# Kernel tuning notes

Hardware: AMD Instinct MI355X
Metric: run time of the kernel (lower is better)

The kernel has to match this reference:

```python
import jax, jax.numpy as jnp
import numpy as np

B, O, L, E = 8, 4, 1024, 1024
BETA = 512
NSEG = 12
OUT = 1


def setup_inputs() -> dict:
    key = jax.random.key(0)
    ks = jax.random.split(key, 8)
    hidden = jax.random.normal(ks[0], (B, O, L, E), jnp.float32)
    # strictly increasing boundaries in (1, L), shared across the O options (as in the torch code)
    raw = jnp.sort(jax.random.randint(ks[1], (B, NSEG), 2, L - NSEG), axis=-1)
    idx = raw + jnp.arange(NSEG, dtype=raw.dtype)
    s = 0.02
    Wp = jax.random.normal(ks[2], (E, 2 * BETA), jnp.float32) * s
    bp = jnp.zeros((2 * BETA,), jnp.float32)
    Wa0 = jax.random.normal(ks[3], (2 * BETA, BETA), jnp.float32) * s
    ba0 = jnp.zeros((BETA,), jnp.float32)
    Wa = jax.random.normal(ks[4], (BETA, BETA), jnp.float32) * s
    ba = jnp.zeros((BETA,), jnp.float32)
    Wl0 = jax.random.normal(ks[5], (8 * BETA, BETA), jnp.float32) * s
    bl0 = jnp.zeros((BETA,), jnp.float32)
    Wl = jax.random.normal(ks[6], (BETA, OUT), jnp.float32) * s
    bl = jnp.zeros((OUT,), jnp.float32)
    return dict(hidden=hidden, idx=idx, Wp=Wp, bp=bp, Wa0=Wa0, ba0=ba0,
                Wa=Wa, ba=ba, Wl0=Wl0, bl0=bl0, Wl=Wl, bl=bl)


def _seg_mean(P, starts, ends):
    # P: [B,O,L+1,E] exclusive prefix sums; starts/ends: [B,K] token offsets.
    s = jnp.take_along_axis(P, starts[:, None, :, None], axis=2)
    e = jnp.take_along_axis(P, ends[:, None, :, None], axis=2)
    cnt = (ends - starts).astype(P.dtype)[:, None, :, None]
    return (e - s) / cnt  # [B,O,K,E]


def _get_param(x, Wp, bp):
    e = 1.0 + jax.nn.relu(x @ Wp + bp)
    a, b = jnp.split(e, 2, axis=-1)
    return a, b


def _attn_pool(a, b, Wa0, ba0, Wa, ba):
    # attention-weighted reduction over axis -2 (the 'logic' operator)
    h = jax.nn.relu(jnp.concatenate([a, b], axis=-1) @ Wa0 + ba0)
    w = jax.nn.softmax(h @ Wa + ba, axis=-2)
    return (w * a).sum(axis=-2), (w * b).sum(axis=-2)


def reference(hidden, idx, Wp, bp, Wa0, ba0, Wa, ba, Wl0, bl0, Wl, bl):
    # ---- init_embed: ragged segment means via prefix sums (one pass, no host syncs)
    P = jnp.concatenate([jnp.zeros_like(hidden[:, :, :1]),
                         jnp.cumsum(hidden, axis=2)], axis=2)  # [B,O,L+1,E]
    ones = jnp.ones((idx.shape[0], 1), idx.dtype)
    starts_c = jnp.concatenate([ones, idx[:, :NSEG - 3]], axis=1)  # [B, NSEG-2]
    ends_c = idx[:, :NSEG - 2]
    ctx = _seg_mean(P, starts_c, ends_c)                                # [B,O,Nc,E]
    q = _seg_mean(P, idx[:, NSEG - 3:NSEG - 2], idx[:, NSEG - 2:NSEG - 1])[:, :, 0]
    o = _seg_mean(P, idx[:, NSEG - 2:NSEG - 1], idx[:, NSEG - 1:NSEG])[:, :, 0]
    allc = _seg_mean(P, ones, idx[:, NSEG - 3:NSEG - 2])[:, :, 0]       # [B,O,E]
    # ---- beta params for context segments
    a_c, b_c = _get_param(ctx, Wp, bp)                                  # [B,O,Nc,BETA]
    # intersection over segments
    ia, ib = _attn_pool(a_c, b_c, Wa0, ba0, Wa, ba)                     # [B,O,BETA]
    # renew: pair each segment with the intersection, pool over the pair axis
    pa = jnp.stack([a_c, jnp.broadcast_to(ia[:, :, None, :], a_c.shape)], axis=-2)
    pb = jnp.stack([b_c, jnp.broadcast_to(ib[:, :, None, :], b_c.shape)], axis=-2)
    na, nb = _attn_pool(pa, pb, Wa0, ba0, Wa, ba)                       # [B,O,Nc,BETA]
    # union: invert, attention-pool over segments, invert back
    ua, ub = _attn_pool(1.0 / na, 1.0 / nb, Wa0, ba0, Wa, ba)
    ua, ub = 1.0 / ua, 1.0 / ub                                         # [B,O,BETA]
    # ---- beta params for question / option / whole-context spans
    a_q, b_q = _get_param(q, Wp, bp)
    a_o, b_o = _get_param(o, Wp, bp)
    a_ac, b_ac = _get_param(allc, Wp, bp)
    # ---- classify head: concat 4 beta embeddings -> 8*BETA -> MLP -> logits
    cat = jnp.concatenate([ua, ub, a_ac, b_ac, a_o, b_o, a_q, b_q], axis=-1)
    h = jax.nn.relu(cat @ Wl0 + bl0)
    return h @ Wl + bl  # [B,O,OUT]
```

## Files before the change

### kernel.cpp

```cpp
#include <hip/hip_runtime.h>
#include <hip/hip_bf16.h>

#define B_    8
#define O_    4
#define L_    1024
#define E_    1024
#define BETA_ 512
#define NSEG_ 12
#define BO_   32
#define NCH_  16

enum : size_t {
  WS_SPART = 0,
  WS_X     = WS_SPART + (size_t)BO_ * NCH_ * 12 * E_,
  WS_P1P   = WS_X     + (size_t)BO_ * 13 * E_,
  WS_H1P   = WS_P1P   + (size_t)8  * BO_ * 13 * E_,
  WS_T1P   = WS_H1P   + (size_t)16 * BO_ * 10 * BETA_,
  WS_H2P   = WS_T1P   + (size_t)8  * BO_ * 10 * BETA_,
  WS_T2P   = WS_H2P   + (size_t)8  * BO_ * BETA_,
  WS_H3P   = WS_T2P   + (size_t)8  * BO_ * BETA_,
  WS_T3P   = WS_H3P   + (size_t)16 * BO_ * 10 * BETA_,
  WS_HFP   = WS_T3P   + (size_t)8  * BO_ * 10 * BETA_,
  WS_TE    = WS_HFP   + (size_t)32 * BO_ * BETA_,
  WS_T1B   = WS_TE    + (size_t)BO_ * 13 * E_,
  WS_IAB   = WS_T1B   + (size_t)BO_ * 10 * BETA_,
  WS_RN    = WS_IAB   + (size_t)BO_ * 2 * BETA_,
  WS_CAT   = WS_RN    + (size_t)BO_ * 10 * E_,
  WS_END   = WS_CAT   + (size_t)BO_ * 8 * BETA_,
};

__device__ __forceinline__ float relu_(float v) { return v > 0.f ? v : 0.f; }

__global__ void k1_segsum(const float* __restrict__ hidden, const int* __restrict__ idx,
                          float* __restrict__ Spart) {
    const int chunk = blockIdx.x;
    const int bo = blockIdx.y;
    const int b = bo >> 2;
    int cuts[13];
    cuts[0] = 1;
#pragma unroll
    for (int i = 0; i < 12; ++i) cuts[i + 1] = idx[b * NSEG_ + i];
    const int e4 = threadIdx.x << 2;
    float* sp = Spart + ((size_t)(bo * NCH_ + chunk) * 12) * E_ + e4;
    const float4 z = make_float4(0.f, 0.f, 0.f, 0.f);
#pragma unroll
    for (int m = 0; m < 12; ++m) *reinterpret_cast<float4*>(sp + (size_t)m * E_) = z;
    const int l0 = chunk * 64;
    const int l1 = l0 + 64;
    int lo = l0 < 1 ? 1 : l0;
    const int hi = l1 < cuts[12] ? l1 : cuts[12];
    if (lo >= hi) return;
    const float* base = hidden + (size_t)bo * (L_ * E_) + e4;
    int j = 0;
    while (j < 11 && cuts[j + 1] <= lo) ++j;
    int l = lo;
    while (l < hi) {
        const int e2 = (j < 11 && cuts[j + 1] < hi) ? cuts[j + 1] : hi;
        float sx = 0.f, sy = 0.f, sz = 0.f, sw = 0.f;
        float tx = 0.f, ty = 0.f, tz = 0.f, tw = 0.f;
        for (; l + 1 < e2; l += 2) {
            const float4 v0 = *reinterpret_cast<const float4*>(base + (size_t)l * E_);
            const float4 v1 = *reinterpret_cast<const float4*>(base + (size_t)(l + 1) * E_);
            sx += v0.x; sy += v0.y; sz += v0.z; sw += v0.w;
            tx += v1.x; ty += v1.y; tz += v1.z; tw += v1.w;
        }
        if (l < e2) {
            const float4 v = *reinterpret_cast<const float4*>(base + (size_t)l * E_);
            sx += v.x; sy += v.y; sz += v.z; sw += v.w;
            ++l;
        }
        float4 s; s.x = sx + tx; s.y = sy + ty; s.z = sz + tz; s.w = sw + tw;
        *reinterpret_cast<float4*>(sp + (size_t)j * E_) = s;
        ++j;
    }
}

__global__ __launch_bounds__(256) void k2_means(
    const float* __restrict__ Spart, const int* __restrict__ idx,
    float* __restrict__ X) {
    const int bo = blockIdx.y;
    const int col = blockIdx.x * 256 + threadIdx.x;
    const int b = bo >> 2;
    int cuts[13];
    cuts[0] = 1;
#pragma unroll
    for (int i = 0; i < 12; ++i) cuts[i + 1] = idx[b * NSEG_ + i];
    const float* sp = Spart + (size_t)bo * NCH_ * 12 * E_ + col;
    float allc = 0.f;
#pragma unroll
    for (int m = 0; m < 12; ++m) {
        float s = 0.f;
#pragma unroll
        for (int ch = 0; ch < NCH_; ++ch) s += sp[((size_t)ch * 12 + m) * E_];
        X[((size_t)bo * 13 + m) * E_ + col] = s / (float)(cuts[m + 1] - cuts[m]);
        if (m < 10) allc += s;
    }
    X[((size_t)bo * 13 + 12) * E_ + col] = allc / (float)(cuts[10] - 1);
}

template<int M, int ML, int K, int N, int KC, int BOG, int XF, int NPART>
__global__ __launch_bounds__(256) void gemm_sk(
    const float* __restrict__ Xb, const float* __restrict__ xbias,
    const float* __restrict__ W, float* __restrict__ OUT,
    const float* __restrict__ A0, const float* __restrict__ A1,
    const float* __restrict__ A2, const float* __restrict__ A3,
    float* __restrict__ SIDE, float* __restrict__ SIDE2) {
    const int kidx = blockIdx.x;
    const int k0 = kidx * KC;
    const int bo0 = blockIdx.y * BOG;
    const int c = blockIdx.z * 256 + threadIdx.x;
    const int tid = threadIdx.x;
    __shared__ __align__(16) float xs[BOG * ML * KC];

    for (int i = tid; i < BOG * ML * KC; i += 256) {
        const int kk = i % KC;
        const int rm = i / KC;
        const int m = rm % ML;
        const int bb = rm / ML;
        const int bo = bo0 + bb;
        const int k = k0 + kk;
        float v;
        if constexpr (XF == 0) {
            v = Xb[((size_t)bo * ML + m) * K + k];
        } else if constexpr (XF == 1) {
            float s = xbias[k];
#pragma unroll
            for (int p = 0; p < NPART; ++p)
                s += Xb[(((size_t)p * BO_ + bo) * ML + m) * K + k];
            v = 1.f + relu_(s);
            SIDE[((size_t)bo * ML + m) * K + k] = v;
        } else if constexpr (XF == 2) {
            float s = xbias[k];
#pragma unroll
            for (int p = 0; p < NPART; ++p)
                s += Xb[(((size_t)p * BO_ + bo) * ML + m) * K + k];
            v = relu_(s);
        } else {
            const int col = k & 511, half = k >> 9;
            const float tj = A0[((size_t)bo * 10 + m) * BETA_ + col];
            float tI = A2[col];
#pragma unroll
            for (int p = 0; p < NPART; ++p)
                tI += A1[((size_t)p * BO_ + bo) * BETA_ + col];
            const float mx = fmaxf(tj, tI);
            const float e0 = expf(tj - mx);
            const float e1 = expf(tI - mx);
            const float ea = A3[((size_t)bo * 13 + m) * E_ + half * BETA_ + col];
            const float iv = SIDE2[(size_t)bo * 1024 + k];
            v = (e0 + e1) / (e0 * ea + e1 * iv);
            SIDE[((size_t)bo * 10 + m) * E_ + k] = v;
        }
        xs[i] = v;
    }
    __syncthreads();

    float acc[BOG][M];
#pragma unroll
    for (int b = 0; b < BOG; ++b)
#pragma unroll
        for (int m = 0; m < M; ++m) acc[b][m] = 0.f;
    const float* __restrict__ wp = W + (size_t)k0 * N + c;
    for (int k4 = 0; k4 < KC / 4; ++k4) {
        const float w0 = wp[(size_t)(4 * k4 + 0) * N];
        const float w1 = wp[(size_t)(4 * k4 + 1) * N];
        const float w2 = wp[(size_t)(4 * k4 + 2) * N];
        const float w3 = wp[(size_t)(4 * k4 + 3) * N];
#pragma unroll
        for (int b = 0; b < BOG; ++b) {
#pragma unroll
            for (int m = 0; m < M; ++m) {
                const float4 xv = *reinterpret_cast<const float4*>(&xs[(b * ML + m) * KC + 4 * k4]);
                float a = acc[b][m];
                a = fmaf(xv.x, w0, a);
                a = fmaf(xv.y, w1, a);
                a = fmaf(xv.z, w2, a);
                a = fmaf(xv.w, w3, a);
                acc[b][m] = a;
            }
        }
    }
#pragma unroll
    for (int b = 0; b < BOG; ++b) {
        float* op = OUT + (((size_t)kidx * BO_ + bo0 + b) * M) * N + c;
#pragma unroll
        for (int m = 0; m < M; ++m) op[(size_t)m * N] = acc[b][m];
    }
}

__global__ void __launch_bounds__(128) t_iab(
    const float* __restrict__ T1P, const float* __restrict__ ba,
    const float* __restrict__ TE, float* __restrict__ T1B,
    float* __restrict__ IAB) {
    const int bo = blockIdx.x;
    const int c = blockIdx.y * 128 + threadIdx.x;
    const float bac = ba[c];
    float t[10], mx = -1e30f;
#pragma unroll
    for (int j = 0; j < 10; ++j) {
        float s = bac;
#pragma unroll
        for (int p = 0; p < 8; ++p)
            s += T1P[(((size_t)p * BO_ + bo) * 10 + j) * BETA_ + c];
        t[j] = s;
        T1B[((size_t)bo * 10 + j) * BETA_ + c] = s;
        mx = fmaxf(mx, s);
    }
    float p[10], sw = 0.f;
#pragma unroll
    for (int j = 0; j < 10; ++j) { p[j] = expf(t[j] - mx); sw += p[j]; }
    float ia = 0.f, ib = 0.f;
#pragma unroll
    for (int j = 0; j < 10; ++j) {
        ia = fmaf(p[j], TE[((size_t)bo * 13 + j) * E_ + c], ia);
        ib = fmaf(p[j], TE[((size_t)bo * 13 + j) * E_ + BETA_ + c], ib);
    }
    IAB[(size_t)bo * 1024 + c] = ia / sw;
    IAB[(size_t)bo * 1024 + BETA_ + c] = ib / sw;
}

__global__ __launch_bounds__(256) void t_cat(
    const float* __restrict__ T3P, const float* __restrict__ ba,
    const float* __restrict__ RN, const float* __restrict__ TE,
    float* __restrict__ CAT) {
    const int bo = blockIdx.y;
    const int k = blockIdx.x * 256 + threadIdx.x;
    float v;
    if (k < 1024) {
        const int col = k & 511;
        const float bac = ba[col];
        float t[10], mx = -1e30f;
#pragma unroll
        for (int j = 0; j < 10; ++j) {
            float s = bac;
#pragma unroll
            for (int p = 0; p < 8; ++p)
                s += T3P[(((size_t)p * BO_ + bo) * 10 + j) * BETA_ + col];
            t[j] = s;
            mx = fmaxf(mx, s);
        }
        float sw = 0.f, acc = 0.f;
#pragma unroll
        for (int j = 0; j < 10; ++j) {
            const float pj = expf(t[j] - mx);
            sw += pj;
            acc = fmaf(pj, RN[((size_t)bo * 10 + j) * E_ + k], acc);
        }
        v = sw / acc;
    } else {
        const int region = k >> 10;
        const int row = (region == 1) ? 12 : (region == 2) ? 11 : 10;
        v = TE[((size_t)bo * 13 + row) * E_ + (k & 1023)];
    }
    CAT[(size_t)bo * 4096 + k] = v;
}

__global__ void __launch_bounds__(512) k_final(
    const float* __restrict__ HFP, const float* __restrict__ bl0,
    const float* __restrict__ Wl, const float* __restrict__ bl,
    float* __restrict__ out) {
    const int bo = blockIdx.x;
    const int c = threadIdx.x;
    float s = bl0[c];
#pragma unroll
    for (int p = 0; p < 32; ++p) s += HFP[((size_t)p * BO_ + bo) * BETA_ + c];
    float partial = relu_(s) * Wl[c];
#pragma unroll
    for (int off = 32; off > 0; off >>= 1) partial += __shfl_down(partial, off, 64);
    __shared__ float red[8];
    if ((c & 63) == 0) red[c >> 6] = partial;
    __syncthreads();
    if (c == 0) out[bo] = red[0] + red[1] + red[2] + red[3] + red[4] + red[5] + red[6] + red[7] + bl[0];
}

extern "C" void kernel_launch(void* const* d_in, const int* in_sizes, int n_in,
                              void* d_out, int out_size, void* d_ws, size_t ws_size,
                              hipStream_t stream) {
    const float* hidden = (const float*)d_in[0];
    const int* idx = (const int*)d_in[1];
    const float* Wp  = (const float*)d_in[2];
    const float* bp  = (const float*)d_in[3];
    const float* Wa0 = (const float*)d_in[4];
    const float* ba0 = (const float*)d_in[5];
    const float* Wa  = (const float*)d_in[6];
    const float* ba  = (const float*)d_in[7];
    const float* Wl0 = (const float*)d_in[8];
    const float* bl0 = (const float*)d_in[9];
    const float* Wl  = (const float*)d_in[10];
    const float* bl  = (const float*)d_in[11];
    float* ws = (float*)d_ws;
    float* SPART = ws + WS_SPART;
    float* X     = ws + WS_X;
    float* P1P   = ws + WS_P1P;
    float* H1P   = ws + WS_H1P;
    float* T1P   = ws + WS_T1P;
    float* H2P   = ws + WS_H2P;
    float* T2P   = ws + WS_T2P;
    float* H3P   = ws + WS_H3P;
    float* T3P   = ws + WS_T3P;
    float* HFP   = ws + WS_HFP;
    float* TE    = ws + WS_TE;
    float* T1B   = ws + WS_T1B;
    float* IAB   = ws + WS_IAB;
    float* RN    = ws + WS_RN;
    float* CAT   = ws + WS_CAT;
    const float* NUL = nullptr;

    k1_segsum<<<dim3(NCH_, BO_), 256, 0, stream>>>(hidden, idx, SPART);
    k2_means<<<dim3(4, BO_), 256, 0, stream>>>(SPART, idx, X);
    gemm_sk<13, 13, 1024, 1024, 128, 2, 0, 1>
        <<<dim3(8, 16, 4), 256, 0, stream>>>(X, NUL, Wp, P1P, NUL, NUL, NUL, NUL, nullptr, nullptr);
    gemm_sk<10, 13, 1024, 512, 64, 2, 1, 8>
        <<<dim3(16, 16, 2), 256, 0, stream>>>(P1P, bp, Wa0, H1P, NUL, NUL, NUL, NUL, TE, nullptr);
    gemm_sk<10, 10, 512, 512, 64, 2, 2, 16>
        <<<dim3(8, 16, 2), 256, 0, stream>>>(H1P, ba0, Wa, T1P, NUL, NUL, NUL, NUL, nullptr, nullptr);
    t_iab<<<dim3(BO_, 4), 128, 0, stream>>>(T1P, ba, TE, T1B, IAB);
    gemm_sk<1, 1, 1024, 512, 128, 8, 0, 1>
        <<<dim3(8, 4, 2), 256, 0, stream>>>(IAB, NUL, Wa0, H2P, NUL, NUL, NUL, NUL, nullptr, nullptr);
    gemm_sk<1, 1, 512, 512, 64, 8, 2, 8>
        <<<dim3(8, 4, 2), 256, 0, stream>>>(H2P, ba0, Wa, T2P, NUL, NUL, NUL, NUL, nullptr, nullptr);
    gemm_sk<10, 10, 1024, 512, 64, 2, 5, 8>
        <<<dim3(16, 16, 2), 256, 0, stream>>>(NUL, NUL, Wa0, H3P, T1B, T2P, ba, TE, RN, IAB);
    gemm_sk<10, 10, 512, 512, 64, 2, 2, 16>
        <<<dim3(8, 16, 2), 256, 0, stream>>>(H3P, ba0, Wa, T3P, NUL, NUL, NUL, NUL, nullptr, nullptr);
    t_cat<<<dim3(16, BO_), 256, 0, stream>>>(T3P, ba, RN, TE, CAT);
    gemm_sk<1, 1, 4096, 512, 128, 8, 0, 1>
        <<<dim3(32, 4, 2), 256, 0, stream>>>(CAT, NUL, Wl0, HFP, NUL, NUL, NUL, NUL, nullptr, nullptr);
    k_final<<<BO_, 512, 0, stream>>>(HFP, bl0, Wl, bl, (float*)d_out);
}
```

Baseline: 160.2 us.

## Fuse segment-mean reduction into first GEMM load and skip zeroing partials

Removes the k2_means kernel. The first projection GEMM now reads the per-chunk partial sums directly and reduces only the chunks that overlap each segment, using precomputed reciprocal counts. Because only overlapping chunks are read, k1 no longer zero-fills its partial buffers. It also retunes the split-K factors of the small H2 and final classifier GEMMs, changing the partial counts and workspace sizes to match. The trade-off is that the reduction is now recomputed inside the GEMM tiles, once per column-block of the grid, instead of being done once.

Result: no change. 161.5 us (+0.8%).

```diff
diff --git a/kernel.cpp b/kernel.cpp
--- a/kernel.cpp
+++ b/kernel.cpp
@@ -12,16 +12,15 @@
 
 enum : size_t {
   WS_SPART = 0,
-  WS_X     = WS_SPART + (size_t)BO_ * NCH_ * 12 * E_,
-  WS_P1P   = WS_X     + (size_t)BO_ * 13 * E_,
+  WS_P1P   = WS_SPART + (size_t)BO_ * NCH_ * 12 * E_,
   WS_H1P   = WS_P1P   + (size_t)8  * BO_ * 13 * E_,
   WS_T1P   = WS_H1P   + (size_t)16 * BO_ * 10 * BETA_,
   WS_H2P   = WS_T1P   + (size_t)8  * BO_ * 10 * BETA_,
-  WS_T2P   = WS_H2P   + (size_t)8  * BO_ * BETA_,
+  WS_T2P   = WS_H2P   + (size_t)16 * BO_ * BETA_,
   WS_H3P   = WS_T2P   + (size_t)8  * BO_ * BETA_,
   WS_T3P   = WS_H3P   + (size_t)16 * BO_ * 10 * BETA_,
   WS_HFP   = WS_T3P   + (size_t)8  * BO_ * 10 * BETA_,
-  WS_TE    = WS_HFP   + (size_t)32 * BO_ * BETA_,
+  WS_TE    = WS_HFP   + (size_t)16 * BO_ * BETA_,
   WS_T1B   = WS_TE    + (size_t)BO_ * 13 * E_,
   WS_IAB   = WS_T1B   + (size_t)BO_ * 10 * BETA_,
   WS_RN    = WS_IAB   + (size_t)BO_ * 2 * BETA_,
@@ -40,17 +39,14 @@
     cuts[0] = 1;
 #pragma unroll
     for (int i = 0; i < 12; ++i) cuts[i + 1] = idx[b * NSEG_ + i];
-    const int e4 = threadIdx.x << 2;
-    float* sp = Spart + ((size_t)(bo * NCH_ + chunk) * 12) * E_ + e4;
-    const float4 z = make_float4(0.f, 0.f, 0.f, 0.f);
-#pragma unroll
-    for (int m = 0; m < 12; ++m) *reinterpret_cast<float4*>(sp + (size_t)m * E_) = z;
     const int l0 = chunk * 64;
     const int l1 = l0 + 64;
     int lo = l0 < 1 ? 1 : l0;
     const int hi = l1 < cuts[12] ? l1 : cuts[12];
     if (lo >= hi) return;
+    const int e4 = threadIdx.x << 2;
     const float* base = hidden + (size_t)bo * (L_ * E_) + e4;
+    float* sp = Spart + ((size_t)(bo * NCH_ + chunk) * 12) * E_ + e4;
     int j = 0;
     while (j < 11 && cuts[j + 1] <= lo) ++j;
     int l = lo;
@@ -75,42 +71,32 @@
     }
 }
 
-__global__ __launch_bounds__(256) void k2_means(
-    const float* __restrict__ Spart, const int* __restrict__ idx,
-    float* __restrict__ X) {
-    const int bo = blockIdx.y;
-    const int col = blockIdx.x * 256 + threadIdx.x;
-    const int b = bo >> 2;
-    int cuts[13];
-    cuts[0] = 1;
-#pragma unroll
-    for (int i = 0; i < 12; ++i) cuts[i + 1] = idx[b * NSEG_ + i];
-    const float* sp = Spart + (size_t)bo * NCH_ * 12 * E_ + col;
-    float allc = 0.f;
-#pragma unroll
-    for (int m = 0; m < 12; ++m) {
-        float s = 0.f;
-#pragma unroll
-        for (int ch = 0; ch < NCH_; ++ch) s += sp[((size_t)ch * 12 + m) * E_];
-        X[((size_t)bo * 13 + m) * E_ + col] = s / (float)(cuts[m + 1] - cuts[m]);
-        if (m < 10) allc += s;
-    }
-    X[((size_t)bo * 13 + 12) * E_ + col] = allc / (float)(cuts[10] - 1);
-}
-
 template<int M, int ML, int K, int N, int KC, int BOG, int XF, int NPART>
 __global__ __launch_bounds__(256) void gemm_sk(
     const float* __restrict__ Xb, const float* __restrict__ xbias,
     const float* __restrict__ W, float* __restrict__ OUT,
     const float* __restrict__ A0, const float* __restrict__ A1,
     const float* __restrict__ A2, const float* __restrict__ A3,
-    float* __restrict__ SIDE, float* __restrict__ SIDE2) {
+    float* __restrict__ SIDE, float* __restrict__ SIDE2,
+    const int* __restrict__ idxp) {
     const int kidx = blockIdx.x;
     const int k0 = kidx * KC;
     const int bo0 = blockIdx.y * BOG;
     const int c = blockIdx.z * 256 + threadIdx.x;
     const int tid = threadIdx.x;
     __shared__ __align__(16) float xs[BOG * ML * KC];
+
+    int cuts[13];
+    float invc[13];
+    if constexpr (XF == 3) {
+        cuts[0] = 1;
+        const int b0 = bo0 >> 2;
+#pragma unroll
+        for (int i = 0; i < 12; ++i) cuts[i + 1] = idxp[b0 * NSEG_ + i];
+#pragma unroll
+        for (int m = 0; m < 12; ++m) invc[m] = 1.0f / (float)(cuts[m + 1] - cuts[m]);
+        invc[12] = 1.0f / (float)(cuts[10] - 1);
+    }
 
     for (int i = tid; i < BOG * ML * KC; i += 256) {
         const int kk = i % KC;
@@ -122,6 +108,22 @@
         float v;
         if constexpr (XF == 0) {
             v = Xb[((size_t)bo * ML + m) * K + k];
+        } else if constexpr (XF == 3) {
+            const float* sp = Xb + (size_t)bo * NCH_ * 12 * E_ + k;
+            float s = 0.f;
+            if (m < 12) {
+                const int c0 = cuts[m] >> 6;
+                const int c1 = (cuts[m + 1] - 1) >> 6;
+                for (int ch = c0; ch <= c1; ++ch) s += sp[((size_t)ch * 12 + m) * E_];
+            } else {
+#pragma unroll
+                for (int r = 0; r < 10; ++r) {
+                    const int c0 = cuts[r] >> 6;
+                    const int c1 = (cuts[r + 1] - 1) >> 6;
+                    for (int ch = c0; ch <= c1; ++ch) s += sp[((size_t)ch * 12 + r) * E_];
+                }
+            }
+            v = s * invc[m];
         } else if constexpr (XF == 1) {
             float s = xbias[k];
 #pragma unroll
@@ -262,7 +264,7 @@
     const int c = threadIdx.x;
     float s = bl0[c];
 #pragma unroll
-    for (int p = 0; p < 32; ++p) s += HFP[((size_t)p * BO_ + bo) * BETA_ + c];
+    for (int p = 0; p < 16; ++p) s += HFP[((size_t)p * BO_ + bo) * BETA_ + c];
     float partial = relu_(s) * Wl[c];
 #pragma unroll
     for (int off = 32; off > 0; off >>= 1) partial += __shfl_down(partial, off, 64);
@@ -289,7 +291,6 @@
     const float* bl  = (const float*)d_in[11];
     float* ws = (float*)d_ws;
     float* SPART = ws + WS_SPART;
-    float* X     = ws + WS_X;
     float* P1P   = ws + WS_P1P;
     float* H1P   = ws + WS_H1P;
     float* T1P   = ws + WS_T1P;
@@ -306,24 +307,23 @@
     const float* NUL = nullptr;
 
     k1_segsum<<<dim3(NCH_, BO_), 256, 0, stream>>>(hidden, idx, SPART);
-    k2_means<<<dim3(4, BO_), 256, 0, stream>>>(SPART, idx, X);
-    gemm_sk<13, 13, 1024, 1024, 128, 2, 0, 1>
-        <<<dim3(8, 16, 4), 256, 0, stream>>>(X, NUL, Wp, P1P, NUL, NUL, NUL, NUL, nullptr, nullptr);
+    gemm_sk<13, 13, 1024, 1024, 128, 2, 3, 1>
+        <<<dim3(8, 16, 4), 256, 0, stream>>>(SPART, NUL, Wp, P1P, NUL, NUL, NUL, NUL, nullptr, nullptr, idx);
     gemm_sk<10, 13, 1024, 512, 64, 2, 1, 8>
-        <<<dim3(16, 16, 2), 256, 0, stream>>>(P1P, bp, Wa0, H1P, NUL, NUL, NUL, NUL, TE, nullptr);
+        <<<dim3(16, 16, 2), 256, 0, stream>>>(P1P, bp, Wa0, H1P, NUL, NUL, NUL, NUL, TE, nullptr, nullptr);
     gemm_sk<10, 10, 512, 512, 64, 2, 2, 16>
-        <<<dim3(8, 16, 2), 256, 0, stream>>>(H1P, ba0, Wa, T1P, NUL, NUL, NUL, NUL, nullptr, nullptr);
+        <<<dim3(8, 16, 2), 256, 0, stream>>>(H1P, ba0, Wa, T1P, NUL, NUL, NUL, NUL, nullptr, nullptr, nullptr);
     t_iab<<<dim3(BO_, 4), 128, 0, stream>>>(T1P, ba, TE, T1B, IAB);
-    gemm_sk<1, 1, 1024, 512, 128, 8, 0, 1>
-        <<<dim3(8, 4, 2), 256, 0, stream>>>(IAB, NUL, Wa0, H2P, NUL, NUL, NUL, NUL, nullptr, nullptr);
-    gemm_sk<1, 1, 512, 512, 64, 8, 2, 8>
-        <<<dim3(8, 4, 2), 256, 0, stream>>>(H2P, ba0, Wa, T2P, NUL, NUL, NUL, NUL, nullptr, nullptr);
+    gemm_sk<1, 1, 1024, 512, 64, 8, 0, 1>
+        <<<dim3(16, 4, 2), 256, 0, stream>>>(IAB, NUL, Wa0, H2P, NUL, NUL, NUL, NUL, nullptr, nullptr, nullptr);
+    gemm_sk<1, 1, 512, 512, 64, 8, 2, 16>
+        <<<dim3(8, 4, 2), 256, 0, stream>>>(H2P, ba0, Wa, T2P, NUL, NUL, NUL, NUL, nullptr, nullptr, nullptr);
     gemm_sk<10, 10, 1024, 512, 64, 2, 5, 8>
-        <<<dim3(16, 16, 2), 256, 0, stream>>>(NUL, NUL, Wa0, H3P, T1B, T2P, ba, TE, RN, IAB);
+        <<<dim3(16, 16, 2), 256, 0, stream>>>(NUL, NUL, Wa0, H3P, T1B, T2P, ba, TE, RN, IAB, nullptr);
     gemm_sk<10, 10, 512, 512, 64, 2, 2, 16>
-        <<<dim3(8, 16, 2), 256, 0, stream>>>(H3P, ba0, Wa, T3P, NUL, NUL, NUL, NUL, nullptr, nullptr);
+        <<<dim3(8, 16, 2), 256, 0, stream>>>(H3P, ba0, Wa, T3P, NUL, NUL, NUL, NUL, nullptr, nullptr, nullptr);
     t_cat<<<dim3(16, BO_), 256, 0, stream>>>(T3P, ba, RN, TE, CAT);
-    gemm_sk<1, 1, 4096, 512, 128, 8, 0, 1>
-        <<<dim3(32, 4, 2), 256, 0, stream>>>(CAT, NUL, Wl0, HFP, NUL, NUL, NUL, NUL, nullptr, nullptr);
+    gemm_sk<1, 1, 4096, 512, 256, 8, 0, 1>
+        <<<dim3(16, 4, 2), 256, 0, stream>>>(CAT, NUL, Wl0, HFP, NUL, NUL, NUL, NUL, nullptr, nullptr, nullptr);
     k_final<<<BO_, 512, 0, stream>>>(HFP, bl0, Wl, bl, (float*)d_out);
 }
```
